# Optimization experiments

Measured on AMD Instinct MI355X. Metric: run time of the kernel, lower is better.

The kernel has to match this reference:

```python
import jax, jax.numpy as jnp
import numpy as np

EPS = 1e-8

def leaky(x):
    return jnp.where(x >= 0, x, 0.1 * x)

def gln(y, gamma, beta, axes):
    # global layer norm: normalize over all non-batch axes given
    mean = jnp.mean(y, axis=axes, keepdims=True)
    var = jnp.mean((y - mean) ** 2, axis=axes, keepdims=True)
    return gamma * (y - mean) / jnp.sqrt(var + EPS) + beta

def conv1d(x, w, b, stride, padding):
    # x: [N, Cin, T], w: [Cout, Cin, K]
    out = jax.lax.conv_general_dilated(
        x, w, window_strides=(stride,), padding=[(padding, padding)],
        dimension_numbers=('NCH', 'OIH', 'NCH'))
    return out + b[None, :, None]

def setup_inputs() -> dict:
    key = jax.random.key(0)
    ks = jax.random.split(key, 8)
    M, C, B, T = 4, 2, 128, 2000
    feature = jax.random.normal(ks[0], (M, B, T), jnp.float32)
    mask = jax.random.uniform(ks[1], (M, C, B, T), jnp.float32)
    # Conv2d(B*C -> 1, 1x1) weight stored as [C, B] (xavier-ish scale)
    w2d = jax.random.normal(ks[2], (C, B), jnp.float32) * (1.0 / np.sqrt(C * B))
    b2d = jnp.zeros((), jnp.float32)
    g2d = jnp.ones((), jnp.float32)    # GLN_2D(1) gamma
    be2d = jnp.zeros((), jnp.float32)  # GLN_2D(1) beta
    # Conv1d stack: 128->256 (k3,s2,p1), 256->256 (k3,s2,p1), 256->1 (k1,s1)
    w1 = jax.random.normal(ks[3], (256, B, 3), jnp.float32) * (1.0 / np.sqrt(B * 3))
    b1 = jnp.zeros((256,), jnp.float32)
    g1 = jnp.ones((1, 256, 1), jnp.float32)
    bb1 = jnp.zeros((1, 256, 1), jnp.float32)
    w2 = jax.random.normal(ks[4], (256, 256, 3), jnp.float32) * (1.0 / np.sqrt(256 * 3))
    b2 = jnp.zeros((256,), jnp.float32)
    g2 = jnp.ones((1, 256, 1), jnp.float32)
    bb2 = jnp.zeros((1, 256, 1), jnp.float32)
    w3 = jax.random.normal(ks[5], (1, 256, 1), jnp.float32) * (1.0 / np.sqrt(256))
    b3 = jnp.zeros((1,), jnp.float32)
    return dict(feature=feature, mask=mask, w2d=w2d, b2d=b2d, g2d=g2d, be2d=be2d,
                w1=w1, b1=b1, g1=g1, bb1=bb1, w2=w2, b2=b2, g2=g2, bb2=bb2,
                w3=w3, b3=b3)

def reference(feature, mask, w2d, b2d, g2d, be2d,
              w1, b1, g1, bb1, w2, b2, g2, bb2, w3, b3):
    # torch: d_in = einsum('bft,bcpt->bcfpt').view(B, C*F, P, T) -> Conv2d(C*F->1, 1x1)
    # With F == P == B, the viewed channel index is (c*F + f), so the 1x1 conv is
    #   d[b,p,t] = sum_{c,f} w2d[c,f] * feature[b,f,t] * mask[b,c,p,t] + b2d
    # expressed as a fused two-step contraction (same math, no 5D materialization):
    a = jnp.einsum('cf,bft->bct', w2d, feature)        # [M, C, T]
    d = jnp.einsum('bct,bcpt->bpt', a, mask) + b2d     # [M, P, T]
    d = d[:, None]                                     # [M, 1, P, T]
    d = gln(d, g2d, be2d, axes=(1, 2, 3))              # GLN_2D(1)
    d = leaky(d)
    x = d[:, 0]                                        # squeeze(1) -> [M, B, T]
    x = leaky(gln(conv1d(x, w1, b1, 2, 1), g1, bb1, (1, 2)))
    x = leaky(gln(conv1d(x, w2, b2, 2, 1), g2, bb2, (1, 2)))
    x = conv1d(x, w3, b3, 1, 0)                        # [M, 1, 500]
    return x
```

## Files before the change

kernel.cpp:

```cpp
#include <hip/hip_runtime.h>
#include <hip/hip_bf16.h>

#define EPS 1e-8f
typedef unsigned short ushortT;
typedef __bf16 bf16x8 __attribute__((ext_vector_type(8)));
typedef float f32x4 __attribute__((ext_vector_type(4)));
union B8 { uint4 u; bf16x8 v; };

__device__ __forceinline__ float leaky(float x) { return x >= 0.f ? x : 0.1f * x; }

__device__ __forceinline__ ushortT f2bf(float v) {
    unsigned u = __float_as_uint(v);
    return (ushortT)((u + 0x7fffu + ((u >> 16) & 1u)) >> 16);
}

__device__ __forceinline__ void block_reduce2(float& s, float& q, float* red) {
    __syncthreads();
    #pragma unroll
    for (int off = 32; off > 0; off >>= 1) {
        s += __shfl_down(s, off, 64);
        q += __shfl_down(q, off, 64);
    }
    const int wid = threadIdx.x >> 6, lane = threadIdx.x & 63;
    if (lane == 0) { red[wid] = s; red[4 + wid] = q; }
    __syncthreads();
    if (threadIdx.x == 0) {
        s = red[0] + red[1] + red[2] + red[3];
        q = red[4] + red[5] + red[6] + red[7];
    }
}

__device__ __forceinline__ void stats_from_partials(const float* __restrict__ partials,
                                                    int n, float nrm,
                                                    float* red, float* stat) {
    float s = 0.f, q = 0.f;
    if ((int)threadIdx.x < n) {
        s = partials[threadIdx.x * 2];
        q = partials[threadIdx.x * 2 + 1];
    }
    block_reduce2(s, q, red);
    if (threadIdx.x == 0) {
        float mean = s * nrm;
        float var  = fmaxf(q * nrm - mean * mean, 0.f);
        stat[0] = mean;
        stat[1] = rsqrtf(var + EPS);
    }
    __syncthreads();
}

__global__ void ka(const float* __restrict__ feature, const float* __restrict__ mask,
                   const float* __restrict__ w2d, const float* __restrict__ b2d,
                   const float* __restrict__ w1, const float* __restrict__ w2,
                   ushortT* __restrict__ w1b, ushortT* __restrict__ w2b,
                   float* __restrict__ dT, float* __restrict__ p0out) {
    if (blockIdx.x >= 128) {
        int p = (blockIdx.x - 128) * 4 + blockIdx.y;
        int base = (p < 96 ? p : p - 96) * 1024 + threadIdx.x * 4;
        const float* src = (p < 96) ? (w1 + base) : (w2 + base);
        ushortT* dst = (p < 96) ? (w1b + base) : (w2b + base);
        float4 v = *(const float4*)src;
        ushort4 o;
        o.x = f2bf(v.x); o.y = f2bf(v.y); o.z = f2bf(v.z); o.w = f2bf(v.w);
        *(ushort4*)dst = o;
        return;
    }
    __shared__ float apart[4][2][64];
    __shared__ float a0s[64], a1s[64];
    __shared__ float Xt[64][33];
    __shared__ float red[8];
    const int b = blockIdx.y;
    const int tile = blockIdx.x >> 2, pt = blockIdx.x & 3;
    const int t0 = tile * 64, p0 = pt * 32;
    const int tc = threadIdx.x & 63, fg = threadIdx.x >> 6;
    const int t = t0 + tc;

    float s0 = 0.f, s1 = 0.f;
    if (t < 2000) {
        const float* fb = feature + ((size_t)b * 128 + fg * 32) * 2000 + t;
        const float* wa = w2d + fg * 32;
        const float* wc = w2d + 128 + fg * 32;
        #pragma unroll
        for (int i = 0; i < 32; i++) {
            float fv = fb[i * 2000];
            s0 = fmaf(wa[i], fv, s0);
            s1 = fmaf(wc[i], fv, s1);
        }
    }
    apart[fg][0][tc] = s0;
    apart[fg][1][tc] = s1;
    __syncthreads();
    if (threadIdx.x < 128) {
        int c = threadIdx.x >> 6, tt = threadIdx.x & 63;
        float s = apart[0][c][tt] + apart[1][c][tt] + apart[2][c][tt] + apart[3][c][tt];
        (c ? a1s : a0s)[tt] = s;
    }
    __syncthreads();

    const float bb = b2d[0];
    float s = 0.f, q = 0.f;
    if (t < 2000) {
        const float a0 = a0s[tc], a1 = a1s[tc];
        const float* m0p = mask + ((size_t)(b * 2 + 0) * 128 + p0) * 2000 + t;
        const float* m1p = mask + ((size_t)(b * 2 + 1) * 128 + p0) * 2000 + t;
        #pragma unroll
        for (int pass = 0; pass < 8; pass++) {
            int pl = fg + pass * 4;
            float v = fmaf(a0, m0p[(size_t)pl * 2000], a1 * m1p[(size_t)pl * 2000]) + bb;
            Xt[tc][pl] = v;
            s += v; q = fmaf(v, v, q);
        }
    }
    block_reduce2(s, q, red);
    if (threadIdx.x == 0) {
        p0out[(b * 128 + blockIdx.x) * 2]     = s;
        p0out[(b * 128 + blockIdx.x) * 2 + 1] = q;
    }
    const int lane8 = threadIdx.x & 7, tr0 = threadIdx.x >> 3;
    #pragma unroll
    for (int pass = 0; pass < 2; pass++) {
        int tr = tr0 + pass * 32;
        if (t0 + tr < 2000) {
            float4 v = { Xt[tr][lane8 * 4], Xt[tr][lane8 * 4 + 1],
                         Xt[tr][lane8 * 4 + 2], Xt[tr][lane8 * 4 + 3] };
            *(float4*)(dT + (size_t)b * 256000 + (size_t)(t0 + tr) * 128 + p0 + lane8 * 4) = v;
        }
    }
}

template <int CIN, int TIN, int TOUT, int NT, bool PERCH, bool TOUT_TRANS>
__launch_bounds__(256, 2)
__global__ void kconv(const float* __restrict__ xT, const float* __restrict__ pin,
                      float nrm,
                      const float* __restrict__ gam, const float* __restrict__ bet,
                      const ushortT* __restrict__ wb, const float* __restrict__ bias,
                      float* __restrict__ yout, float* __restrict__ pout) {
    constexpr int K = CIN * 3;
    constexpr int ROWB = K * 2;
    constexpr int NF = NT / 16;
    constexpr int LPR = CIN / 4;
    constexpr int RPP = 256 / LPR;
    constexpr int NPASS = (2 * NT + RPP) / RPP;
    __shared__ char Xs[NT * ROWB];
    __shared__ float red[8];
    __shared__ float stat[2];

    const int b = blockIdx.y;
    const int ms = blockIdx.x & 3;
    const int tile = blockIdx.x >> 2;
    const int t0 = tile * NT;
    const int lane = threadIdx.x & 63;
    const int wv = threadIdx.x >> 6;

    stats_from_partials(pin + b * 256, 128, nrm, red, stat);
    const float mean = stat[0], inv = stat[1];

    const int rl = threadIdx.x / LPR;
    const int f0 = (threadIdx.x % LPR) * 4;
    float gg[4], bv[4];
    if (PERCH) {
        float4 g4 = *(const float4*)(gam + f0);
        float4 b4 = *(const float4*)(bet + f0);
        gg[0] = g4.x; gg[1] = g4.y; gg[2] = g4.z; gg[3] = g4.w;
        bv[0] = b4.x; bv[1] = b4.y; bv[2] = b4.z; bv[3] = b4.w;
    } else {
        gg[0] = gg[1] = gg[2] = gg[3] = gam[0];
        bv[0] = bv[1] = bv[2] = bv[3] = bet[0];
    }
    const int base_ti = 2 * t0 - 1;
    #pragma unroll
    for (int pass = 0; pass < NPASS; pass++) {
        int c = pass * RPP + rl;
        if (c > 2 * NT) continue;
        int ti = base_ti + c;
        float4 x4 = {0.f, 0.f, 0.f, 0.f};
        if (ti >= 0 && ti < TIN)
            x4 = *(const float4*)(xT + ((size_t)b * TIN + ti) * CIN + f0);
        float xv[4] = {x4.x, x4.y, x4.z, x4.w};
        ushortT h[4];
        #pragma unroll
        for (int j = 0; j < 4; j++)
            h[j] = f2bf(leaky(fmaf(gg[j] * inv, xv[j] - mean, bv[j])));
        if (c & 1) {
            int tt = (c - 1) >> 1;
            int ad = tt * ROWB, sw = (tt & 7) << 4;
            #pragma unroll
            for (int j = 0; j < 4; j++)
                *(ushortT*)(Xs + ((ad + ((f0 + j) * 3 + 1) * 2) ^ sw)) = h[j];
        } else {
            int tt = c >> 1;
            if (tt < NT) {
                int ad = tt * ROWB, sw = (tt & 7) << 4;
                #pragma unroll
                for (int j = 0; j < 4; j++)
                    *(ushortT*)(Xs + ((ad + (f0 + j) * 6) ^ sw)) = h[j];
            }
            if (tt >= 1) {
                int ad = (tt - 1) * ROWB, sw = ((tt - 1) & 7) << 4;
                #pragma unroll
                for (int j = 0; j < 4; j++)
                    *(ushortT*)(Xs + ((ad + (f0 + j) * 6 + 4) ^ sw)) = h[j];
            }
        }
    }
    __syncthreads();

    const int obase = ms * 64 + wv * 16;
    const int kgrp = (lane >> 4) * 8;
    const int mrow = lane & 15;
    f32x4 acc[NF];
    #pragma unroll
    for (int nf = 0; nf < NF; nf++) acc[nf] = (f32x4){0.f, 0.f, 0.f, 0.f};
    #pragma unroll 2
    for (int ks = 0; ks < K / 32; ks++) {
        int kb = ks * 32 + kgrp;
        B8 afr;
        afr.u = *(const uint4*)(wb + (size_t)(obase + mrow) * K + kb);
        #pragma unroll
        for (int nf = 0; nf < NF; nf++) {
            int tt = nf * 16 + mrow;
            int ad = (tt * ROWB + kb * 2) ^ ((tt & 7) << 4);
            B8 bfr; bfr.u = *(const uint4*)(Xs + ad);
            acc[nf] = __builtin_amdgcn_mfma_f32_16x16x32_bf16(afr.v, bfr.v, acc[nf], 0, 0, 0);
        }
    }

    float s = 0.f, q = 0.f;
    if (TOUT_TRANS) {
        const int o0 = obase + (lane >> 4) * 4;
        float4 b4 = *(const float4*)(bias + o0);
        float bi[4] = {b4.x, b4.y, b4.z, b4.w};
        #pragma unroll
        for (int nf = 0; nf < NF; nf++) {
            int t = t0 + nf * 16 + mrow;
            if (t < TOUT) {
                float v0 = acc[nf][0] + bi[0], v1 = acc[nf][1] + bi[1];
                float v2 = acc[nf][2] + bi[2], v3 = acc[nf][3] + bi[3];
                float4 v = {v0, v1, v2, v3};
                *(float4*)(yout + ((size_t)b * TOUT + t) * 256 + o0) = v;
                s += v0 + v1 + v2 + v3;
                q = fmaf(v0, v0, q); q = fmaf(v1, v1, q);
                q = fmaf(v2, v2, q); q = fmaf(v3, v3, q);
            }
        }
    } else {
        const int o0 = obase + (lane >> 4) * 4;
        #pragma unroll
        for (int nf = 0; nf < NF; nf++) {
            int t = t0 + nf * 16 + mrow;
            if (t < TOUT) {
                #pragma unroll
                for (int r = 0; r < 4; r++) {
                    float v = acc[nf][r] + bias[o0 + r];
                    yout[((size_t)b * 256 + o0 + r) * TOUT + t] = v;
                    s += v; q = fmaf(v, v, q);
                }
            }
        }
    }
    block_reduce2(s, q, red);
    if (threadIdx.x == 0) {
        int bi = b * 128 + tile * 4 + ms;
        pout[bi * 2]     = s;
        pout[bi * 2 + 1] = q;
    }
}

__global__ void kd_head(const float* __restrict__ y2, const float* __restrict__ p2,
                        const float* __restrict__ g2, const float* __restrict__ bb2,
                        const float* __restrict__ w3, const float* __restrict__ b3,
                        float* __restrict__ out) {
    __shared__ float red[8];
    __shared__ float stat[2];
    __shared__ float part[4][64];
    const int b = blockIdx.y;
    stats_from_partials(p2 + b * 256, 128, 1.f / 128000.f, red, stat);
    const float mean = stat[0], inv = stat[1];
    const int tl = threadIdx.x & 63, fg = threadIdx.x >> 6;
    const int t = blockIdx.x * 64 + tl;
    float acc = 0.f;
    if (t < 500) {
        const float* yb = y2 + ((size_t)b * 256 + fg * 64) * 500 + t;
        #pragma unroll 8
        for (int i = 0; i < 64; i++) {
            int o = fg * 64 + i;
            float raw = yb[i * 500];
            float xv = leaky(fmaf(g2[o] * inv, raw - mean, bb2[o]));
            acc = fmaf(w3[o], xv, acc);
        }
    }
    part[fg][tl] = acc;
    __syncthreads();
    if (fg == 0 && t < 500)
        out[b * 500 + t] = b3[0] + part[0][tl] + part[1][tl] + part[2][tl] + part[3][tl];
}

extern "C" void kernel_launch(void* const* d_in, const int* in_sizes, int n_in,
                              void* d_out, int out_size, void* d_ws, size_t ws_size,
                              hipStream_t stream) {
    const float* feature = (const float*)d_in[0];
    const float* mask    = (const float*)d_in[1];
    const float* w2d     = (const float*)d_in[2];
    const float* b2d     = (const float*)d_in[3];
    const float* g2d     = (const float*)d_in[4];
    const float* be2d    = (const float*)d_in[5];
    const float* w1      = (const float*)d_in[6];
    const float* b1      = (const float*)d_in[7];
    const float* g1      = (const float*)d_in[8];
    const float* bb1     = (const float*)d_in[9];
    const float* w2      = (const float*)d_in[10];
    const float* b2      = (const float*)d_in[11];
    const float* g2      = (const float*)d_in[12];
    const float* bb2     = (const float*)d_in[13];
    const float* w3      = (const float*)d_in[14];
    const float* b3      = (const float*)d_in[15];
    float* out = (float*)d_out;

    float* ws = (float*)d_ws;
    float* p0  = ws;
    float* p1  = ws + 1024;
    float* p2  = ws + 2048;
    float* dT  = ws + 3072;
    float* y1T = dT + 1024000;
    float* y2  = y1T + 1024000;
    ushortT* w1b = (ushortT*)(y2 + 512000);
    ushortT* w2b = w1b + 98304;

    ka<<<dim3(128 + 72, 4), 256, 0, stream>>>(feature, mask, w2d, b2d,
                                              w1, w2, w1b, w2b, dT, p0);
    kconv<128, 2000, 1000, 32, false, true><<<dim3(128, 4), 256, 0, stream>>>(
        dT, p0, 1.f / 256000.f, g2d, be2d, w1b, b1, y1T, p1);
    kconv<256, 1000, 500, 16, true, false><<<dim3(128, 4), 256, 0, stream>>>(
        y1T, p1, 1.f / 256000.f, g1, bb1, w2b, b2, y2, p2);
    kd_head<<<dim3(8, 4), 256, 0, stream>>>(y2, p2, g2, bb2, w3, b3, out);
}
```

Before: 43.34 us.

## Retile first stage over all channels with float4 loads; register-block conv1 outputs

The first kernel now gives each block a 32-timestep tile across all 128 output channels. It uses float4 loads of feature and mask, so the channel mix `a` is computed once per timestep instead of once per four-channel-group block. The first conv is retiled to 16 timesteps by 128 output channels per block, with each wave holding two MFMA row fragments so one loaded activation fragment is reused twice. Partial-statistic counts become a runtime parameter to match the new block counts. The cost is more accumulator registers in conv1 and fewer, larger blocks in the first kernel, which may reduce latency hiding.

```diff
diff --git a/kernel.cpp b/kernel.cpp
--- a/kernel.cpp
+++ b/kernel.cpp
@@ -53,8 +53,8 @@
                    const float* __restrict__ w1, const float* __restrict__ w2,
                    ushortT* __restrict__ w1b, ushortT* __restrict__ w2b,
                    float* __restrict__ dT, float* __restrict__ p0out) {
-    if (blockIdx.x >= 128) {
-        int p = (blockIdx.x - 128) * 4 + blockIdx.y;
+    if (blockIdx.x >= 63) {
+        int p = (blockIdx.x - 63) * 4 + blockIdx.y;
         int base = (p < 96 ? p : p - 96) * 1024 + threadIdx.x * 4;
         const float* src = (p < 96) ? (w1 + base) : (w2 + base);
         ushortT* dst = (p < 96) ? (w1b + base) : (w2b + base);
@@ -64,50 +64,74 @@
         *(ushort4*)dst = o;
         return;
     }
-    __shared__ float apart[4][2][64];
-    __shared__ float a0s[64], a1s[64];
-    __shared__ float Xt[64][33];
+    __shared__ float4 apart[2][32][8];
+    __shared__ float4 a0s4[8], a1s4[8];
+    __shared__ float Xt[32][132];
     __shared__ float red[8];
     const int b = blockIdx.y;
-    const int tile = blockIdx.x >> 2, pt = blockIdx.x & 3;
-    const int t0 = tile * 64, p0 = pt * 32;
-    const int tc = threadIdx.x & 63, fg = threadIdx.x >> 6;
-    const int t = t0 + tc;
-
-    float s0 = 0.f, s1 = 0.f;
-    if (t < 2000) {
-        const float* fb = feature + ((size_t)b * 128 + fg * 32) * 2000 + t;
-        const float* wa = w2d + fg * 32;
-        const float* wc = w2d + 128 + fg * 32;
+    const int t0 = blockIdx.x * 32;
+    const int tq = threadIdx.x & 7;
+    const int hi = threadIdx.x >> 3;
+
+    {
+        const int tbase = t0 + tq * 4;
+        float4 s0 = {0.f, 0.f, 0.f, 0.f}, s1 = s0;
+        if (tbase + 3 < 2000) {
+            const float* fb = feature + ((size_t)b * 128 + hi * 4) * 2000 + tbase;
+            float4 wa = *(const float4*)(w2d + hi * 4);
+            float4 wc = *(const float4*)(w2d + 128 + hi * 4);
+            float wav[4] = {wa.x, wa.y, wa.z, wa.w};
+            float wcv[4] = {wc.x, wc.y, wc.z, wc.w};
+            #pragma unroll
+            for (int i = 0; i < 4; i++) {
+                float4 fv = *(const float4*)(fb + (size_t)i * 2000);
+                s0.x = fmaf(wav[i], fv.x, s0.x); s0.y = fmaf(wav[i], fv.y, s0.y);
+                s0.z = fmaf(wav[i], fv.z, s0.z); s0.w = fmaf(wav[i], fv.w, s0.w);
+                s1.x = fmaf(wcv[i], fv.x, s1.x); s1.y = fmaf(wcv[i], fv.y, s1.y);
+                s1.z = fmaf(wcv[i], fv.z, s1.z); s1.w = fmaf(wcv[i], fv.w, s1.w);
+            }
+        }
+        apart[0][hi][tq] = s0;
+        apart[1][hi][tq] = s1;
+    }
+    __syncthreads();
+    if (threadIdx.x < 16) {
+        int c = threadIdx.x >> 3, tqq = threadIdx.x & 7;
+        float4 s = {0.f, 0.f, 0.f, 0.f};
         #pragma unroll
         for (int i = 0; i < 32; i++) {
-            float fv = fb[i * 2000];
-            s0 = fmaf(wa[i], fv, s0);
-            s1 = fmaf(wc[i], fv, s1);
-        }
-    }
-    apart[fg][0][tc] = s0;
-    apart[fg][1][tc] = s1;
-    __syncthreads();
-    if (threadIdx.x < 128) {
-        int c = threadIdx.x >> 6, tt = threadIdx.x & 63;
-        float s = apart[0][c][tt] + apart[1][c][tt] + apart[2][c][tt] + apart[3][c][tt];
-        (c ? a1s : a0s)[tt] = s;
+            float4 v = apart[c][i][tqq];
+            s.x += v.x; s.y += v.y; s.z += v.z; s.w += v.w;
+        }
+        (c ? a1s4 : a0s4)[tqq] = s;
     }
     __syncthreads();
 
     const float bb = b2d[0];
     float s = 0.f, q = 0.f;
-    if (t < 2000) {
-        const float a0 = a0s[tc], a1 = a1s[tc];
-        const float* m0p = mask + ((size_t)(b * 2 + 0) * 128 + p0) * 2000 + t;
-        const float* m1p = mask + ((size_t)(b * 2 + 1) * 128 + p0) * 2000 + t;
-        #pragma unroll
-        for (int pass = 0; pass < 8; pass++) {
-            int pl = fg + pass * 4;
-            float v = fmaf(a0, m0p[(size_t)pl * 2000], a1 * m1p[(size_t)pl * 2000]) + bb;
-            Xt[tc][pl] = v;
-            s += v; q = fmaf(v, v, q);
+    {
+        const int tbase = t0 + tq * 4;
+        if (tbase + 3 < 2000) {
+            float4 a0 = a0s4[tq], a1 = a1s4[tq];
+            const float* m0p = mask + ((size_t)(b * 2 + 0) * 128 + hi * 4) * 2000 + tbase;
+            const float* m1p = mask + ((size_t)(b * 2 + 1) * 128 + hi * 4) * 2000 + tbase;
+            #pragma unroll
+            for (int j = 0; j < 4; j++) {
+                int p = hi * 4 + j;
+                float4 m0 = *(const float4*)(m0p + (size_t)j * 2000);
+                float4 m1 = *(const float4*)(m1p + (size_t)j * 2000);
+                float v0 = fmaf(a0.x, m0.x, a1.x * m1.x) + bb;
+                float v1 = fmaf(a0.y, m0.y, a1.y * m1.y) + bb;
+                float v2 = fmaf(a0.z, m0.z, a1.z * m1.z) + bb;
+                float v3 = fmaf(a0.w, m0.w, a1.w * m1.w) + bb;
+                Xt[tq * 4 + 0][p] = v0;
+                Xt[tq * 4 + 1][p] = v1;
+                Xt[tq * 4 + 2][p] = v2;
+                Xt[tq * 4 + 3][p] = v3;
+                s += v0 + v1 + v2 + v3;
+                q = fmaf(v0, v0, q); q = fmaf(v1, v1, q);
+                q = fmaf(v2, v2, q); q = fmaf(v3, v3, q);
+            }
         }
     }
     block_reduce2(s, q, red);
@@ -115,43 +139,47 @@
         p0out[(b * 128 + blockIdx.x) * 2]     = s;
         p0out[(b * 128 + blockIdx.x) * 2 + 1] = q;
     }
-    const int lane8 = threadIdx.x & 7, tr0 = threadIdx.x >> 3;
-    #pragma unroll
-    for (int pass = 0; pass < 2; pass++) {
-        int tr = tr0 + pass * 32;
-        if (t0 + tr < 2000) {
-            float4 v = { Xt[tr][lane8 * 4], Xt[tr][lane8 * 4 + 1],
-                         Xt[tr][lane8 * 4 + 2], Xt[tr][lane8 * 4 + 3] };
-            *(float4*)(dT + (size_t)b * 256000 + (size_t)(t0 + tr) * 128 + p0 + lane8 * 4) = v;
-        }
-    }
-}
-
-template <int CIN, int TIN, int TOUT, int NT, bool PERCH, bool TOUT_TRANS>
+    {
+        const int tw = threadIdx.x >> 3;
+        if (t0 + tw < 2000) {
+            float* drow = dT + (size_t)b * 256000 + (size_t)(t0 + tw) * 128;
+            #pragma unroll
+            for (int jj = 0; jj < 4; jj++) {
+                int p4 = (threadIdx.x & 7) + jj * 8;
+                float4 v = *(const float4*)&Xt[tw][p4 * 4];
+                *(float4*)(drow + p4 * 4) = v;
+            }
+        }
+    }
+}
+
+template <int CIN, int TIN, int TOUT, int NT, int MPB, bool PERCH, bool TOUT_TRANS>
 __launch_bounds__(256, 2)
 __global__ void kconv(const float* __restrict__ xT, const float* __restrict__ pin,
-                      float nrm,
+                      int npin, float nrm,
                       const float* __restrict__ gam, const float* __restrict__ bet,
                       const ushortT* __restrict__ wb, const float* __restrict__ bias,
                       float* __restrict__ yout, float* __restrict__ pout) {
     constexpr int K = CIN * 3;
     constexpr int ROWB = K * 2;
     constexpr int NF = NT / 16;
+    constexpr int MSC = 256 / MPB;
+    constexpr int MF = MPB / 64;
     constexpr int LPR = CIN / 4;
     constexpr int RPP = 256 / LPR;
-    constexpr int NPASS = (2 * NT + RPP) / RPP;
+    constexpr int NPASS = (2 * NT) / RPP + 1;
     __shared__ char Xs[NT * ROWB];
     __shared__ float red[8];
     __shared__ float stat[2];
 
     const int b = blockIdx.y;
-    const int ms = blockIdx.x & 3;
-    const int tile = blockIdx.x >> 2;
+    const int ms = blockIdx.x % MSC;
+    const int tile = blockIdx.x / MSC;
     const int t0 = tile * NT;
     const int lane = threadIdx.x & 63;
     const int wv = threadIdx.x >> 6;
 
-    stats_from_partials(pin + b * 256, 128, nrm, red, stat);
+    stats_from_partials(pin + b * 256, npin, nrm, red, stat);
     const float mean = stat[0], inv = stat[1];
 
     const int rl = threadIdx.x / LPR;
@@ -204,62 +232,71 @@
     }
     __syncthreads();
 
-    const int obase = ms * 64 + wv * 16;
+    const int obase = ms * MPB + wv * (MPB / 4);
     const int kgrp = (lane >> 4) * 8;
     const int mrow = lane & 15;
-    f32x4 acc[NF];
+    f32x4 acc[MF][NF];
     #pragma unroll
-    for (int nf = 0; nf < NF; nf++) acc[nf] = (f32x4){0.f, 0.f, 0.f, 0.f};
+    for (int mf = 0; mf < MF; mf++)
+        #pragma unroll
+        for (int nf = 0; nf < NF; nf++) acc[mf][nf] = (f32x4){0.f, 0.f, 0.f, 0.f};
     #pragma unroll 2
     for (int ks = 0; ks < K / 32; ks++) {
         int kb = ks * 32 + kgrp;
-        B8 afr;
-        afr.u = *(const uint4*)(wb + (size_t)(obase + mrow) * K + kb);
+        B8 afr[MF];
+        #pragma unroll
+        for (int mf = 0; mf < MF; mf++)
+            afr[mf].u = *(const uint4*)(wb + (size_t)(obase + mf * 16 + mrow) * K + kb);
         #pragma unroll
         for (int nf = 0; nf < NF; nf++) {
             int tt = nf * 16 + mrow;
             int ad = (tt * ROWB + kb * 2) ^ ((tt & 7) << 4);
             B8 bfr; bfr.u = *(const uint4*)(Xs + ad);
-            acc[nf] = __builtin_amdgcn_mfma_f32_16x16x32_bf16(afr.v, bfr.v, acc[nf], 0, 0, 0);
+            #pragma unroll
+            for (int mf = 0; mf < MF; mf++)
+                acc[mf][nf] = __builtin_amdgcn_mfma_f32_16x16x32_bf16(
+                    afr[mf].v, bfr.v, acc[mf][nf], 0, 0, 0);
         }
     }
 
     float s = 0.f, q = 0.f;
-    if (TOUT_TRANS) {
-        const int o0 = obase + (lane >> 4) * 4;
-        float4 b4 = *(const float4*)(bias + o0);
-        float bi[4] = {b4.x, b4.y, b4.z, b4.w};
-        #pragma unroll
-        for (int nf = 0; nf < NF; nf++) {
-            int t = t0 + nf * 16 + mrow;
-            if (t < TOUT) {
-                float v0 = acc[nf][0] + bi[0], v1 = acc[nf][1] + bi[1];
-                float v2 = acc[nf][2] + bi[2], v3 = acc[nf][3] + bi[3];
-                float4 v = {v0, v1, v2, v3};
-                *(float4*)(yout + ((size_t)b * TOUT + t) * 256 + o0) = v;
-                s += v0 + v1 + v2 + v3;
-                q = fmaf(v0, v0, q); q = fmaf(v1, v1, q);
-                q = fmaf(v2, v2, q); q = fmaf(v3, v3, q);
-            }
-        }
-    } else {
-        const int o0 = obase + (lane >> 4) * 4;
-        #pragma unroll
-        for (int nf = 0; nf < NF; nf++) {
-            int t = t0 + nf * 16 + mrow;
-            if (t < TOUT) {
-                #pragma unroll
-                for (int r = 0; r < 4; r++) {
-                    float v = acc[nf][r] + bias[o0 + r];
-                    yout[((size_t)b * 256 + o0 + r) * TOUT + t] = v;
-                    s += v; q = fmaf(v, v, q);
+    #pragma unroll
+    for (int mf = 0; mf < MF; mf++) {
+        const int o0 = obase + mf * 16 + (lane >> 4) * 4;
+        if (TOUT_TRANS) {
+            float4 b4 = *(const float4*)(bias + o0);
+            float bi[4] = {b4.x, b4.y, b4.z, b4.w};
+            #pragma unroll
+            for (int nf = 0; nf < NF; nf++) {
+                int t = t0 + nf * 16 + mrow;
+                if (t < TOUT) {
+                    float v0 = acc[mf][nf][0] + bi[0], v1 = acc[mf][nf][1] + bi[1];
+                    float v2 = acc[mf][nf][2] + bi[2], v3 = acc[mf][nf][3] + bi[3];
+                    float4 v = {v0, v1, v2, v3};
+                    *(float4*)(yout + ((size_t)b * TOUT + t) * 256 + o0) = v;
+                    s += v0 + v1 + v2 + v3;
+                    q = fmaf(v0, v0, q); q = fmaf(v1, v1, q);
+                    q = fmaf(v2, v2, q); q = fmaf(v3, v3, q);
+                }
+            }
+        } else {
+            #pragma unroll
+            for (int nf = 0; nf < NF; nf++) {
+                int t = t0 + nf * 16 + mrow;
+                if (t < TOUT) {
+                    #pragma unroll
+                    for (int r = 0; r < 4; r++) {
+                        float v = acc[mf][nf][r] + bias[o0 + r];
+                        yout[((size_t)b * 256 + o0 + r) * TOUT + t] = v;
+                        s += v; q = fmaf(v, v, q);
+                    }
                 }
             }
         }
     }
     block_reduce2(s, q, red);
     if (threadIdx.x == 0) {
-        int bi = b * 128 + tile * 4 + ms;
+        int bi = b * 128 + tile * MSC + ms;
         pout[bi * 2]     = s;
         pout[bi * 2 + 1] = q;
     }
@@ -325,11 +362,11 @@
     ushortT* w1b = (ushortT*)(y2 + 512000);
     ushortT* w2b = w1b + 98304;
 
-    ka<<<dim3(128 + 72, 4), 256, 0, stream>>>(feature, mask, w2d, b2d,
-                                              w1, w2, w1b, w2b, dT, p0);
-    kconv<128, 2000, 1000, 32, false, true><<<dim3(128, 4), 256, 0, stream>>>(
-        dT, p0, 1.f / 256000.f, g2d, be2d, w1b, b1, y1T, p1);
-    kconv<256, 1000, 500, 16, true, false><<<dim3(128, 4), 256, 0, stream>>>(
-        y1T, p1, 1.f / 256000.f, g1, bb1, w2b, b2, y2, p2);
+    ka<<<dim3(63 + 72, 4), 256, 0, stream>>>(feature, mask, w2d, b2d,
+                                             w1, w2, w1b, w2b, dT, p0);
+    kconv<128, 2000, 1000, 16, 128, false, true><<<dim3(126, 4), 256, 0, stream>>>(
+        dT, p0, 63, 1.f / 256000.f, g2d, be2d, w1b, b1, y1T, p1);
+    kconv<256, 1000, 500, 16, 64, true, false><<<dim3(128, 4), 256, 0, stream>>>(
+        y1T, p1, 126, 1.f / 256000.f, g1, bb1, w2b, b2, y2, p2);
     kd_head<<<dim3(8, 4), 256, 0, stream>>>(y2, p2, g2, bb2, w3, b3, out);
 }
```

Measured after the change: 42.48 us. -2.0%, faster.
